# Performance work log

Measured on AMD Instinct MI355X. Metric: run time of the kernel, lower is better.

Reference implementation:

```python
import jax, jax.numpy as jnp
import numpy as np

D_MODEL = 4096
D_LATENT = 512
NUM_HEADS = 32
HEAD_DIM = D_MODEL // NUM_HEADS  # 128
ROPE_THETA = 10000.0
BATCH, SEQ = 2, 2048


def _rotate_half(x):
    x1, x2 = jnp.split(x, 2, axis=-1)
    return jnp.concatenate([-x2, x1], axis=-1)


def _rope_cos_sin(positions, head_dim, theta, dtype):
    # positions: [B, S] -> cos/sin: [B, S, 1, head_dim]
    inv_freq = 1.0 / (theta ** (jnp.arange(0, head_dim, 2, dtype=jnp.float32) / head_dim))
    freqs = positions.astype(jnp.float32)[..., None] * inv_freq  # [B,S,hd/2]
    emb = jnp.concatenate([freqs, freqs], axis=-1)               # [B,S,hd]
    return jnp.cos(emb)[:, :, None, :].astype(dtype), jnp.sin(emb)[:, :, None, :].astype(dtype)


def setup_inputs() -> dict:
    key = jax.random.key(0)
    ks = jax.random.split(key, 6)
    s = 0.02
    return {
        "hidden_states": jax.random.normal(ks[0], (BATCH, SEQ, D_MODEL), jnp.float32),
        "Wq": jax.random.normal(ks[1], (D_MODEL, NUM_HEADS * HEAD_DIM), jnp.float32) * s,
        "Wc": jax.random.normal(ks[2], (D_MODEL, D_LATENT), jnp.float32) * s,
        "Wk": jax.random.normal(ks[3], (D_LATENT, NUM_HEADS * HEAD_DIM), jnp.float32) * s,
        "Wv": jax.random.normal(ks[4], (D_LATENT, NUM_HEADS * HEAD_DIM), jnp.float32) * s,
        "Wo": jax.random.normal(ks[5], (NUM_HEADS * HEAD_DIM, D_MODEL), jnp.float32) * s,
    }


def reference(hidden_states, Wq, Wc, Wk, Wv, Wo):
    B, S, _ = hidden_states.shape
    H, Dh = NUM_HEADS, HEAD_DIM

    q = (hidden_states @ Wq).reshape(B, S, H, Dh)
    kv_latent = hidden_states @ Wc                     # [B,S,d_latent]
    k = (kv_latent @ Wk).reshape(B, S, H, Dh)
    v = (kv_latent @ Wv).reshape(B, S, H, Dh)

    # RoPE: q uses positions [0..S), k uses positions [0..S) (no past cache)
    pos = jnp.broadcast_to(jnp.arange(S)[None, :], (B, S))
    cos, sin = _rope_cos_sin(pos, Dh, ROPE_THETA, q.dtype)
    q = q * cos + _rotate_half(q) * sin
    k = k * cos + _rotate_half(k) * sin

    # standard attention, no mask (faithful to attention_mask=None path)
    scale = 1.0 / np.sqrt(Dh)
    scores = jnp.einsum("bqhd,bkhd->bhqk", q, k) * scale
    probs = jax.nn.softmax(scores, axis=-1)
    attn = jnp.einsum("bhqk,bkhd->bqhd", probs, v)     # [B,S,H,Dh]

    out = attn.reshape(B, S, H * Dh) @ Wo
    return out
```

## Files before the change

### kernel.cpp

```cpp
#include <hip/hip_runtime.h>
#include <hip/hip_bf16.h>
#include <cstdint>
#include <cstddef>

#define D_MODEL 4096
#define D_LATENT 512
#define NUM_HEADS 32
#define HEAD_DIM 128
#define BATCH 2
#define SEQ 2048
#define ROWS (BATCH*SEQ)

typedef __attribute__((ext_vector_type(8))) short bf16x8;
typedef __attribute__((ext_vector_type(4))) float f32x4;
typedef __attribute__((ext_vector_type(16))) float f32x16;
typedef unsigned int uint;

static __device__ __forceinline__ unsigned short f2bf(float f){
  union { float f; uint32_t u; } v; v.f = f;
  uint32_t r = (v.u + 0x7fffu + ((v.u >> 16) & 1u)) >> 16;
  return (unsigned short)r;
}
static __device__ __forceinline__ float bf2f(unsigned short h){
  union { uint32_t u; float f; } v; v.u = ((uint32_t)h) << 16;
  return v.f;
}
static __device__ __forceinline__ uint cvtpk(float lo, float hi2){
  uint r;
  asm("v_cvt_pk_bf16_f32 %0, %1, %2" : "=v"(r) : "v"(lo), "v"(hi2));
  return r;
}
static __device__ __forceinline__ void gload16(const void* g, void* l){
  __builtin_amdgcn_global_load_lds(
      (const __attribute__((address_space(1))) void*)g,
      (__attribute__((address_space(3))) void*)l, 16, 0, 0);
}

__global__ __launch_bounds__(256) void f32_to_bf16(
    const float* __restrict__ in, unsigned short* __restrict__ out){
  const size_t i = ((size_t)blockIdx.x * 256 + threadIdx.x) * 8;
  const float4 lo = *(const float4*)(in + i);
  const float4 hi = *(const float4*)(in + i + 4);
  uint4 d; unsigned short* dp = (unsigned short*)&d;
  dp[0]=f2bf(lo.x); dp[1]=f2bf(lo.y); dp[2]=f2bf(lo.z); dp[3]=f2bf(lo.w);
  dp[4]=f2bf(hi.x); dp[5]=f2bf(hi.y); dp[6]=f2bf(hi.z); dp[7]=f2bf(hi.w);
  *(uint4*)(out + i) = d;
}

__global__ __launch_bounds__(256) void transpose_convert(
    const float* __restrict__ W, unsigned short* __restrict__ Wt, int K, int N){
  __shared__ float tile[64][65];
  const int k0 = blockIdx.x * 64, n0 = blockIdx.y * 64;
  const int t = threadIdx.x;
  #pragma unroll
  for (int j = 0; j < 16; ++j){
    const int idx = t + 256*j;
    const int r = idx >> 6, c = idx & 63;
    tile[r][c] = W[(size_t)(k0 + r) * N + n0 + c];
  }
  __syncthreads();
  #pragma unroll
  for (int j = 0; j < 16; ++j){
    const int idx = t + 256*j;
    const int r = idx >> 6, c = idx & 63;
    Wt[(size_t)(n0 + r) * K + k0 + c] = f2bf(tile[c][r]);
  }
}

__global__ __launch_bounds__(256) void rope_table_kernel(float* __restrict__ ct,
                                                         float* __restrict__ st){
  const int i = blockIdx.x * 256 + threadIdx.x;
  if (i >= SEQ * 64) return;
  const int s = i >> 6, j = i & 63;
  const float inv = powf(10000.0f, -(float)j / 64.0f);
  const double a = (double)s * (double)inv;
  ct[i] = (float)cos(a);
  st[i] = (float)sin(a);
}

__global__ __launch_bounds__(256) void rope_apply(unsigned short* __restrict__ buf,
    const float* __restrict__ ct, const float* __restrict__ st, float scale){
  const int i = blockIdx.x * 256 + threadIdx.x;
  const int j = i & 63;
  const int tmp = i >> 6;
  const int h = tmp & 31;
  const int row = tmp >> 5;
  const int s = row & (SEQ - 1);
  const float c = ct[s*64 + j], sn = st[s*64 + j];
  const size_t base = (size_t)row * D_MODEL + (size_t)h * 128;
  const float x1 = bf2f(buf[base + j]);
  const float x2 = bf2f(buf[base + j + 64]);
  buf[base + j]      = f2bf((x1 * c - x2 * sn) * scale);
  buf[base + j + 64] = f2bf((x2 * c + x1 * sn) * scale);
}

template<bool OF32>
__global__ __launch_bounds__(256) void gemm_kernel(
    const unsigned short* __restrict__ A, const unsigned short* __restrict__ Bt,
    void* __restrict__ Cp, int M, int N, int K){
  __shared__ __align__(16) char As[128 * 128];
  __shared__ __align__(16) char Bs[128 * 128];
  const int t = threadIdx.x;
  const int nbx = gridDim.x;
  const int nwg = nbx * gridDim.y;
  int bid = blockIdx.y * nbx + blockIdx.x;
  bid = (bid & 7) * (nwg >> 3) + (bid >> 3);
  const int m0 = (bid / nbx) * 128, n0 = (bid % nbx) * 128;
  const int l = t & 63, wid = t >> 6;
  const int wr = wid >> 1, wcn = wid & 1;
  const int lr = l & 15, lg = l >> 4;

  const int srow = l >> 3;
  const int gch  = (l & 7) ^ srow;
  const unsigned short* gA = A  + (size_t)(m0 + wid*32 + srow) * K + gch*8;
  const unsigned short* gB = Bt + (size_t)(n0 + wid*32 + srow) * K + gch*8;
  char* lA = As + wid*4096;
  char* lB = Bs + wid*4096;

  f32x4 acc[4][4];
  #pragma unroll
  for (int i = 0; i < 4; ++i)
    #pragma unroll
    for (int j = 0; j < 4; ++j)
      #pragma unroll
      for (int r = 0; r < 4; ++r) acc[i][j][r] = 0.0f;

  const int kTiles = K >> 6;
  for (int kt = 0; kt < kTiles; ++kt){
    const size_t ko = (size_t)kt << 6;
    #pragma unroll
    for (int i = 0; i < 4; ++i){
      gload16(gA + (size_t)i*8*K + ko, lA + i*1024);
      gload16(gB + (size_t)i*8*K + ko, lB + i*1024);
    }
    __syncthreads();
    #pragma unroll
    for (int kc = 0; kc < 2; ++kc){
      bf16x8 af[4], bfv[4];
      const int ch = kc*4 + lg;
      #pragma unroll
      for (int mb = 0; mb < 4; ++mb){
        const int row = wr*64 + mb*16 + lr;
        af[mb] = *(const bf16x8*)(As + row*128 + ((ch ^ (row & 7)) * 16));
      }
      #pragma unroll
      for (int nb = 0; nb < 4; ++nb){
        const int row = wcn*64 + nb*16 + lr;
        bfv[nb] = *(const bf16x8*)(Bs + row*128 + ((ch ^ (row & 7)) * 16));
      }
      #pragma unroll
      for (int mb = 0; mb < 4; ++mb)
        #pragma unroll
        for (int nb = 0; nb < 4; ++nb)
          acc[mb][nb] = __builtin_amdgcn_mfma_f32_16x16x32_bf16(af[mb], bfv[nb], acc[mb][nb], 0, 0, 0);
    }
    __syncthreads();
  }
  #pragma unroll
  for (int mb = 0; mb < 4; ++mb)
    #pragma unroll
    for (int nb = 0; nb < 4; ++nb)
      #pragma unroll
      for (int r = 0; r < 4; ++r){
        const int row = m0 + wr*64 + mb*16 + lg*4 + r;
        const int col = n0 + wcn*64 + nb*16 + lr;
        if constexpr (OF32) ((float*)Cp)[(size_t)row * N + col] = acc[mb][nb][r];
        else ((unsigned short*)Cp)[(size_t)row * N + col] = f2bf(acc[mb][nb][r]);
      }
}

template<int MH>
static __device__ __forceinline__ void rdAh(bf16x8 (&a_)[4][2], const char* buf,
                                            int wr, int lr, int lg){
  #pragma unroll
  for (int mm = 0; mm < 4; ++mm)
    #pragma unroll
    for (int kc = 0; kc < 2; ++kc){
      const int row = wr*128 + (MH*4 + mm)*16 + lr;
      const int ch = kc*4 + lg;
      a_[mm][kc] = *(const bf16x8*)(buf + row*128 + ((ch ^ (row & 7)) * 16));
    }
}
template<int NH>
static __device__ __forceinline__ void rdBh(bf16x8 (&b_)[2][2][2], const char* buf,
                                            int wc, int lr, int lg){
  #pragma unroll
  for (int nn = 0; nn < 2; ++nn)
    #pragma unroll
    for (int kc = 0; kc < 2; ++kc){
      const int row = wc*64 + (NH*2 + nn)*16 + lr;
      const int ch = kc*4 + lg;
      b_[NH][nn][kc] = *(const bf16x8*)(buf + row*128 + ((ch ^ (row & 7)) * 16));
    }
}
template<int MH, int NH>
static __device__ __forceinline__ void mfq(f32x4 (&acc)[8][4],
    const bf16x8 (&a_)[4][2], const bf16x8 (&b_)[2][2][2]){
  __builtin_amdgcn_s_setprio(1);
  #pragma unroll
  for (int kc = 0; kc < 2; ++kc)
    #pragma unroll
    for (int mm = 0; mm < 4; ++mm)
      #pragma unroll
      for (int nn = 0; nn < 2; ++nn)
        acc[MH*4+mm][NH*2+nn] = __builtin_amdgcn_mfma_f32_16x16x32_bf16(
            a_[mm][kc], b_[NH][nn][kc], acc[MH*4+mm][NH*2+nn], 0, 0, 0);
  __builtin_amdgcn_s_setprio(0);
}

#define G256_BAR  __builtin_amdgcn_s_barrier()
#define G256_LGK0 do{ asm volatile("s_waitcnt lgkmcnt(0)" ::: "memory"); \
                      __builtin_amdgcn_sched_barrier(0); }while(0)
#define G256_VM(n) asm volatile("s_waitcnt vmcnt(" #n ")" ::: "memory")

template<bool OF32>
__global__ __launch_bounds__(512, 2) void gemm256_kernel(
    const unsigned short* __restrict__ A, const unsigned short* __restrict__ Bt,
    void* __restrict__ Cp, void* __restrict__ Cp2, int nsplit, int ldc, int ldc2,
    int M, int N, int K, int vt_mode){
  __shared__ __align__(16) char lds[131072];
  char* const As0 = lds;
  char* const As1 = lds + 32768;
  char* const Bs0 = lds + 65536;
  char* const Bs1 = lds + 98304;

  const int t = threadIdx.x;
  const int l = t & 63, wid = t >> 6;
  const int wr = wid >> 2, wc = wid & 3;
  const int lr = l & 15, lg = l >> 4;
  const int nbx = gridDim.x;
  const int nwg = nbx * gridDim.y;
  int bid = blockIdx.y * nbx + blockIdx.x;
  bid = (bid & 7) * (nwg >> 3) + (bid >> 3);
  const int m0 = (bid / nbx) * 256, n0 = (bid % nbx) * 256;

  const int srow = t >> 3;
  const int pch = t & 7;
  const int gch = pch ^ (srow & 7);
  const unsigned short* gAb = A  + (size_t)(m0 + srow) * K + gch*8;
  const unsigned short* gBb = Bt + (size_t)(n0 + srow) * K + gch*8;
  const int ldso = srow*128 + pch*16;

  auto stA = [&](char* dst, int half, int kcol){
    const unsigned short* g = gAb + (size_t)half*128*K + kcol;
    gload16(g,                dst + half*16384 + ldso);
    gload16(g + (size_t)64*K, dst + half*16384 + 8192 + ldso);
  };
  auto stB = [&](char* dst, int half, int kcol){
    const unsigned short* g = gBb + (size_t)half*128*K + kcol;
    gload16(g,                dst + half*16384 + ldso);
    gload16(g + (size_t)64*K, dst + half*16384 + 8192 + ldso);
  };

  f32x4 acc[8][4];
  #pragma unroll
  for (int m = 0; m < 8; ++m)
    #pragma unroll
    for (int n = 0; n < 4; ++n)
      #pragma unroll
      for (int r = 0; r < 4; ++r) acc[m][n][r] = 0.0f;
  bf16x8 a_[4][2];
  bf16x8 b_[2][2][2];

  const int niter = K >> 7;
  stA(As0, 0, 0); stA(As0, 1, 0); stB(Bs0, 0, 0); stB(Bs0, 1, 0);
  stA(As1, 0, 64);
  G256_VM(2);
  G256_BAR;
  __builtin_amdgcn_sched_barrier(0);

  for (int j = 0; j < niter; ++j){
    const int k0 = j << 7;
    const bool more = (j + 1 < niter);
    rdAh<0>(a_, As0, wr, lr, lg);
    rdBh<0>(b_, Bs0, wc, lr, lg);
    stA(As1, 1, k0 + 64);
    G256_BAR; G256_LGK0;
    mfq<0,0>(acc, a_, b_);
    G256_BAR;
    rdBh<1>(b_, Bs0, wc, lr, lg);
    stB(Bs1, 0, k0 + 64);
    G256_BAR; G256_LGK0;
    mfq<0,1>(acc, a_, b_);
    G256_BAR;
    rdAh<1>(a_, As0, wr, lr, lg);
    stB(Bs1, 1, k0 + 64);
    G256_BAR; G256_LGK0;
    mfq<1,0>(acc, a_, b_);
    G256_BAR;
    if (more){ stA(As0, 0, k0 + 128); G256_VM(2); }
    else     { G256_VM(0); }
    G256_BAR;
    __builtin_amdgcn_sched_barrier(0);
    mfq<1,1>(acc, a_, b_);
    G256_BAR;
    rdAh<0>(a_, As1, wr, lr, lg);
    rdBh<0>(b_, Bs1, wc, lr, lg);
    if (more) stA(As0, 1, k0 + 128);
    G256_BAR; G256_LGK0;
    mfq<0,0>(acc, a_, b_);
    G256_BAR;
    rdBh<1>(b_, Bs1, wc, lr, lg);
    if (more) stB(Bs0, 0, k0 + 128);
    G256_BAR; G256_LGK0;
    mfq<0,1>(acc, a_, b_);
    G256_BAR;
    rdAh<1>(a_, As1, wr, lr, lg);
    if (more) stB(Bs0, 1, k0 + 128);
    G256_BAR; G256_LGK0;
    mfq<1,0>(acc, a_, b_);
    G256_BAR;
    if (more){ stA(As1, 0, k0 + 192); G256_VM(2); }
    G256_BAR;
    __builtin_amdgcn_sched_barrier(0);
    mfq<1,1>(acc, a_, b_);
    G256_BAR;
  }

  if (n0 >= nsplit && vt_mode){
    unsigned short* vtp = (unsigned short*)Cp2;
    #pragma unroll
    for (int m = 0; m < 8; ++m)
      #pragma unroll
      for (int n = 0; n < 4; ++n)
        #pragma unroll
        for (int r = 0; r < 4; ++r){
          const int row = m0 + wr*128 + m*16 + lg*4 + r;
          const int col = (n0 - nsplit) + wc*64 + n*16 + lr;
          const size_t didx = ((size_t)(((row >> 11) << 5) | (col >> 7)) * 128
                               + (col & 127)) * SEQ + (row & (SEQ - 1));
          vtp[didx] = f2bf(acc[m][n][r]);
        }
    return;
  }
  void* outp = Cp;
  int c0 = n0, ld = ldc;
  if (n0 >= nsplit){ outp = Cp2; c0 = n0 - nsplit; ld = ldc2; }
  #pragma unroll
  for (int m = 0; m < 8; ++m)
    #pragma unroll
    for (int n = 0; n < 4; ++n)
      #pragma unroll
      for (int r = 0; r < 4; ++r){
        const int row = m0 + wr*128 + m*16 + lg*4 + r;
        const int col = c0 + wc*64 + n*16 + lr;
        if constexpr (OF32) ((float*)outp)[(size_t)row * ld + col] = acc[m][n][r];
        else ((unsigned short*)outp)[(size_t)row * ld + col] = f2bf(acc[m][n][r]);
      }
}

__global__ __launch_bounds__(512) void attn_kernel(
    const unsigned short* __restrict__ q, const unsigned short* __restrict__ kp,
    const unsigned short* __restrict__ vt, const float* __restrict__ ct,
    const float* __restrict__ st, unsigned short* __restrict__ o){
  __shared__ __align__(16) char Ks[2 * 16384];
  __shared__ __align__(16) char Vs[2 * 16384];
  const int t = threadIdx.x;
  const int l = t & 63, w = t >> 6;
  const int lq = l & 31, hi = l >> 5;
  const int bh = blockIdx.x, qb = blockIdx.y;
  const int b = bh >> 5;
  const size_t qbase = (size_t)b * SEQ + qb*256 + w*32;
  const size_t cb = (size_t)(bh & 31) * 128;

  auto stageK = [&](int buf, int kb){
    const size_t kr0 = (size_t)b * SEQ + (size_t)kb*64;
    char* kdst = Ks + buf*16384 + w*2048;
    #pragma unroll
    for (int i = 0; i < 2; ++i){
      const int r = w*8 + i*4 + (l >> 4);
      const int g = (l & 15) ^ (r & 15);
      gload16(kp + (kr0 + r) * D_MODEL + cb + g*8, kdst + i*1024);
    }
  };
  auto stageV = [&](int buf, int kb){
    char* vdst = Vs + buf*16384 + w*2048;
    #pragma unroll
    for (int i = 0; i < 2; ++i){
      const int r = w*16 + i*8 + (l >> 3);
      const int g = (l & 7) ^ (r & 7);
      gload16(vt + ((size_t)bh*128 + r) * SEQ + (size_t)kb*64 + g*8, vdst + i*1024);
    }
  };

  bf16x8 qf[8];
  #pragma unroll
  for (int dc = 0; dc < 8; ++dc)
    qf[dc] = *(const bf16x8*)(q + (qbase + lq) * D_MODEL + cb + dc*16 + hi*8);
  {
    const float qsc = 0.08838834764831845f * 1.4426950408889634f;
    const int s = qb*256 + w*32 + lq;
    #pragma unroll
    for (int dc = 0; dc < 4; ++dc){
      const int j0 = dc*16 + hi*8;
      const float4 c0 = *(const float4*)(ct + s*64 + j0);
      const float4 c1 = *(const float4*)(ct + s*64 + j0 + 4);
      const float4 s0_ = *(const float4*)(st + s*64 + j0);
      const float4 s1_ = *(const float4*)(st + s*64 + j0 + 4);
      const float cc[8] = {c0.x,c0.y,c0.z,c0.w,c1.x,c1.y,c1.z,c1.w};
      const float ss[8] = {s0_.x,s0_.y,s0_.z,s0_.w,s1_.x,s1_.y,s1_.z,s1_.w};
      #pragma unroll
      for (int e = 0; e < 8; ++e){
        const float x1 = bf2f((unsigned short)qf[dc][e]);
        const float x2 = bf2f((unsigned short)qf[dc + 4][e]);
        qf[dc][e]     = (short)f2bf((x1 * cc[e] - x2 * ss[e]) * qsc);
        qf[dc + 4][e] = (short)f2bf((x2 * cc[e] + x1 * ss[e]) * qsc);
      }
    }
  }

  f32x16 O[4];
  #pragma unroll
  for (int nb = 0; nb < 4; ++nb)
    #pragma unroll
    for (int r = 0; r < 16; ++r) O[nb][r] = 0.0f;
  float m = -1e30f, lsum = 0.0f;

  stageK(0, 0); stageV(0, 0);

  for (int kb = 0; kb < SEQ/64; ++kb){
    const bool more = (kb + 1 < SEQ/64);
    asm volatile("s_waitcnt vmcnt(0)" ::: "memory");
    __builtin_amdgcn_s_barrier();
    __builtin_amdgcn_sched_barrier(0);
    if (more){ stageK((kb + 1) & 1, kb + 1); stageV((kb + 1) & 1, kb + 1); }
    const char* Kb = Ks + (kb & 1)*16384;
    const char* Vb = Vs + (kb & 1)*16384;

    f32x16 s0, s1;
    #pragma unroll
    for (int r = 0; r < 16; ++r){ s0[r] = 0.0f; s1[r] = 0.0f; }
    __builtin_amdgcn_s_setprio(1);
    #pragma unroll
    for (int dc = 0; dc < 8; ++dc){
      const int ch = dc*2 + hi;
      const bf16x8 k0 = *(const bf16x8*)(Kb + lq*256 + ((ch ^ (lq & 15)) * 16));
      const bf16x8 k1 = *(const bf16x8*)(Kb + (32 + lq)*256 + ((ch ^ (lq & 15)) * 16));
      s0 = __builtin_amdgcn_mfma_f32_32x32x16_bf16(k0, qf[dc], s0, 0, 0, 0);
      s1 = __builtin_amdgcn_mfma_f32_32x32x16_bf16(k1, qf[dc], s1, 0, 0, 0);
    }
    __builtin_amdgcn_s_setprio(0);

    float mt = s0[0];
    #pragma unroll
    for (int r = 1; r < 16; ++r) mt = fmaxf(mt, s0[r]);
    #pragma unroll
    for (int r = 0; r < 16; ++r) mt = fmaxf(mt, s1[r]);
    mt = fmaxf(mt, __shfl_xor(mt, 32));

    if (!__all(mt <= m + 8.0f)){
      const float mnew = fmaxf(m, mt);
      const float al = __builtin_amdgcn_exp2f(m - mnew);
      m = mnew;
      lsum *= al;
      #pragma unroll
      for (int r = 0; r < 16; ++r){
        const int crow = (r & 3) + 8*(r >> 2) + 4*hi;
        const float albr = __shfl(al, crow);
        #pragma unroll
        for (int nb = 0; nb < 4; ++nb) O[nb][r] *= albr;
      }
    }

    float E[32];
    float sum = 0.0f;
    #pragma unroll
    for (int r = 0; r < 16; ++r){ E[r] = __builtin_amdgcn_exp2f(s0[r] - m); sum += E[r]; }
    #pragma unroll
    for (int r = 0; r < 16; ++r){ E[16 + r] = __builtin_amdgcn_exp2f(s1[r] - m); sum += E[16 + r]; }
    sum += __shfl_xor(sum, 32);
    lsum += sum;

    bf16x8 pa[4];
    #pragma unroll
    for (int c = 0; c < 4; ++c){
      const int rb = c * 8;
      const uint a_ = cvtpk(E[rb + 0], E[rb + 1]);
      const uint b_ = cvtpk(E[rb + 2], E[rb + 3]);
      const uint c_ = cvtpk(E[rb + 4], E[rb + 5]);
      const uint d_ = cvtpk(E[rb + 6], E[rb + 7]);
      const uint sa = (uint)__shfl_xor((int)a_, 32);
      const uint sb = (uint)__shfl_xor((int)b_, 32);
      const uint sc = (uint)__shfl_xor((int)c_, 32);
      const uint sd = (uint)__shfl_xor((int)d_, 32);
      union { uint u[4]; bf16x8 v; } uu;
      uu.u[0] = hi ? sc : a_;
      uu.u[1] = hi ? sd : b_;
      uu.u[2] = hi ? c_ : sa;
      uu.u[3] = hi ? d_ : sb;
      pa[c] = uu.v;
    }

    __builtin_amdgcn_s_setprio(1);
    #pragma unroll
    for (int c = 0; c < 4; ++c){
      const int ch = c*2 + hi;
      #pragma unroll
      for (int nb = 0; nb < 4; ++nb){
        const int vr = nb*32 + lq;
        const bf16x8 vf = *(const bf16x8*)(Vb + vr*128 + ((ch ^ (vr & 7)) * 16));
        O[nb] = __builtin_amdgcn_mfma_f32_32x32x16_bf16(pa[c], vf, O[nb], 0, 0, 0);
      }
    }
    __builtin_amdgcn_s_setprio(0);
  }

  const float rinv = 1.0f / lsum;
  #pragma unroll
  for (int r = 0; r < 16; ++r){
    const int crow = (r & 3) + 8*(r >> 2) + 4*hi;
    const float rb_ = __shfl(rinv, crow);
    #pragma unroll
    for (int nb = 0; nb < 4; ++nb)
      o[(qbase + crow) * D_MODEL + cb + nb*32 + lq] = f2bf(O[nb][r] * rb_);
  }
}

extern "C" void kernel_launch(void* const* d_in, const int* in_sizes, int n_in,
                              void* d_out, int out_size, void* d_ws, size_t ws_size,
                              hipStream_t stream){
  const float* hidden = (const float*)d_in[0];
  const float* Wq = (const float*)d_in[1];
  const float* Wc = (const float*)d_in[2];
  const float* Wk = (const float*)d_in[3];
  const float* Wv = (const float*)d_in[4];
  const float* Wo = (const float*)d_in[5];
  float* out = (float*)d_out;

  char* ws = (char*)d_ws;
  size_t off = 0;
  auto alloc = [&](size_t bytes)->char*{
    char* p = ws + off; off += (bytes + 255) & ~(size_t)255; return p;
  };
  unsigned short* Wqt  = (unsigned short*)alloc((size_t)D_MODEL * D_MODEL * 2);
  unsigned short* Wct  = (unsigned short*)alloc((size_t)D_LATENT * D_MODEL * 2);
  unsigned short* Wkvt = (unsigned short*)alloc((size_t)2 * D_MODEL * D_LATENT * 2);
  unsigned short* Wot  = (unsigned short*)alloc((size_t)D_MODEL * D_MODEL * 2);
  unsigned short* latent = (unsigned short*)alloc((size_t)ROWS * D_LATENT * 2);
  unsigned short* qbuf = (unsigned short*)alloc((size_t)ROWS * D_MODEL * 2);
  unsigned short* kbuf = (unsigned short*)alloc((size_t)ROWS * D_MODEL * 2);
  unsigned short* attnb= (unsigned short*)alloc((size_t)ROWS * D_MODEL * 2);
  float* ctab = (float*)alloc((size_t)SEQ * 64 * 4);
  float* stab = (float*)alloc((size_t)SEQ * 64 * 4);
  unsigned short* hbf   = attnb;
  unsigned short* vtbuf = Wqt;

  const dim3 B256(256);

  f32_to_bf16<<<(ROWS*(size_t)D_MODEL)/2048, B256, 0, stream>>>(hidden, hbf);
  transpose_convert<<<dim3(64, 64), B256, 0, stream>>>(Wq, Wqt, D_MODEL, D_MODEL);
  transpose_convert<<<dim3(64, 8),  B256, 0, stream>>>(Wc, Wct, D_MODEL, D_LATENT);
  transpose_convert<<<dim3(8, 64),  B256, 0, stream>>>(Wk, Wkvt, D_LATENT, D_MODEL);
  transpose_convert<<<dim3(8, 64),  B256, 0, stream>>>(Wv, Wkvt + (size_t)D_MODEL*D_LATENT, D_LATENT, D_MODEL);
  transpose_convert<<<dim3(64, 64), B256, 0, stream>>>(Wo, Wot, D_MODEL, D_MODEL);
  rope_table_kernel<<<512, B256, 0, stream>>>(ctab, stab);

  gemm_kernel<false><<<dim3(D_LATENT/128, ROWS/128), B256, 0, stream>>>(
      hbf, Wct, latent, ROWS, D_LATENT, D_MODEL);
  gemm256_kernel<false><<<dim3(D_MODEL/256, ROWS/256), dim3(512), 0, stream>>>(
      hbf, Wqt, qbuf, qbuf, 1 << 30, D_MODEL, D_MODEL, ROWS, D_MODEL, D_MODEL, 0);
  gemm256_kernel<false><<<dim3(2*D_MODEL/256, ROWS/256), dim3(512), 0, stream>>>(
      latent, Wkvt, kbuf, vtbuf, D_MODEL, D_MODEL, 0, ROWS, 2*D_MODEL, D_LATENT, 1);

  rope_apply<<<(ROWS * NUM_HEADS * 64) / 256, B256, 0, stream>>>(kbuf, ctab, stab, 1.0f);

  attn_kernel<<<dim3(BATCH * NUM_HEADS, SEQ/256), dim3(512), 0, stream>>>(
      qbuf, kbuf, vtbuf, ctab, stab, attnb);

  gemm256_kernel<true><<<dim3(D_MODEL/256, ROWS/256), dim3(512), 0, stream>>>(
      attnb, Wot, out, out, 1 << 30, D_MODEL, D_MODEL, ROWS, D_MODEL, D_MODEL, 0);
}
```

Before: 609.6 us.

## Split-K the latent projection GEMM and batch weight transposes into fewer launches

```diff
diff --git a/kernel.cpp b/kernel.cpp
--- a/kernel.cpp
+++ b/kernel.cpp
@@ -45,6 +45,30 @@
   dp[0]=f2bf(lo.x); dp[1]=f2bf(lo.y); dp[2]=f2bf(lo.z); dp[3]=f2bf(lo.w);
   dp[4]=f2bf(hi.x); dp[5]=f2bf(hi.y); dp[6]=f2bf(hi.z); dp[7]=f2bf(hi.w);
   *(uint4*)(out + i) = d;
+}
+
+__global__ __launch_bounds__(256) void transpose_convert2(
+    const float* __restrict__ S0, unsigned short* __restrict__ D0,
+    const float* __restrict__ S1, unsigned short* __restrict__ D1,
+    int K, int N){
+  __shared__ float tile[64][65];
+  const float* W = blockIdx.z ? S1 : S0;
+  unsigned short* Wt = blockIdx.z ? D1 : D0;
+  const int k0 = blockIdx.x * 64, n0 = blockIdx.y * 64;
+  const int t = threadIdx.x;
+  #pragma unroll
+  for (int j = 0; j < 16; ++j){
+    const int idx = t + 256*j;
+    const int r = idx >> 6, c = idx & 63;
+    tile[r][c] = W[(size_t)(k0 + r) * N + n0 + c];
+  }
+  __syncthreads();
+  #pragma unroll
+  for (int j = 0; j < 16; ++j){
+    const int idx = t + 256*j;
+    const int r = idx >> 6, c = idx & 63;
+    Wt[(size_t)(n0 + r) * K + k0 + c] = f2bf(tile[c][r]);
+  }
 }
 
 __global__ __launch_bounds__(256) void transpose_convert(
@@ -94,13 +118,13 @@
   buf[base + j + 64] = f2bf((x2 * c + x1 * sn) * scale);
 }
 
-template<bool OF32>
-__global__ __launch_bounds__(256) void gemm_kernel(
+__global__ __launch_bounds__(256) void gemm_splitk_kernel(
     const unsigned short* __restrict__ A, const unsigned short* __restrict__ Bt,
-    void* __restrict__ Cp, int M, int N, int K){
+    float* __restrict__ Cpart, int M, int N, int Kfull, int Kpart){
   __shared__ __align__(16) char As[128 * 128];
   __shared__ __align__(16) char Bs[128 * 128];
   const int t = threadIdx.x;
+  const int kz = blockIdx.z;
   const int nbx = gridDim.x;
   const int nwg = nbx * gridDim.y;
   int bid = blockIdx.y * nbx + blockIdx.x;
@@ -112,8 +136,9 @@
 
   const int srow = l >> 3;
   const int gch  = (l & 7) ^ srow;
-  const unsigned short* gA = A  + (size_t)(m0 + wid*32 + srow) * K + gch*8;
-  const unsigned short* gB = Bt + (size_t)(n0 + wid*32 + srow) * K + gch*8;
+  const size_t kofs = (size_t)kz * Kpart;
+  const unsigned short* gA = A  + (size_t)(m0 + wid*32 + srow) * Kfull + kofs + gch*8;
+  const unsigned short* gB = Bt + (size_t)(n0 + wid*32 + srow) * Kfull + kofs + gch*8;
   char* lA = As + wid*4096;
   char* lB = Bs + wid*4096;
 
@@ -125,13 +150,13 @@
       #pragma unroll
       for (int r = 0; r < 4; ++r) acc[i][j][r] = 0.0f;
 
-  const int kTiles = K >> 6;
+  const int kTiles = Kpart >> 6;
   for (int kt = 0; kt < kTiles; ++kt){
     const size_t ko = (size_t)kt << 6;
     #pragma unroll
     for (int i = 0; i < 4; ++i){
-      gload16(gA + (size_t)i*8*K + ko, lA + i*1024);
-      gload16(gB + (size_t)i*8*K + ko, lB + i*1024);
+      gload16(gA + (size_t)i*8*Kfull + ko, lA + i*1024);
+      gload16(gB + (size_t)i*8*Kfull + ko, lB + i*1024);
     }
     __syncthreads();
     #pragma unroll
@@ -156,6 +181,7 @@
     }
     __syncthreads();
   }
+  float* Cp = Cpart + (size_t)kz * M * N;
   #pragma unroll
   for (int mb = 0; mb < 4; ++mb)
     #pragma unroll
@@ -164,9 +190,21 @@
       for (int r = 0; r < 4; ++r){
         const int row = m0 + wr*64 + mb*16 + lg*4 + r;
         const int col = n0 + wcn*64 + nb*16 + lr;
-        if constexpr (OF32) ((float*)Cp)[(size_t)row * N + col] = acc[mb][nb][r];
-        else ((unsigned short*)Cp)[(size_t)row * N + col] = f2bf(acc[mb][nb][r]);
+        Cp[(size_t)row * N + col] = acc[mb][nb][r];
       }
+}
+
+__global__ __launch_bounds__(256) void latent_reduce(
+    const float* __restrict__ p, unsigned short* __restrict__ out, size_t n){
+  const size_t i = ((size_t)blockIdx.x * 256 + threadIdx.x) * 8;
+  const float4 a0 = *(const float4*)(p + i);
+  const float4 a1 = *(const float4*)(p + i + 4);
+  const float4 b0 = *(const float4*)(p + n + i);
+  const float4 b1 = *(const float4*)(p + n + i + 4);
+  uint4 d; unsigned short* dp = (unsigned short*)&d;
+  dp[0]=f2bf(a0.x+b0.x); dp[1]=f2bf(a0.y+b0.y); dp[2]=f2bf(a0.z+b0.z); dp[3]=f2bf(a0.w+b0.w);
+  dp[4]=f2bf(a1.x+b1.x); dp[5]=f2bf(a1.y+b1.y); dp[6]=f2bf(a1.z+b1.z); dp[7]=f2bf(a1.w+b1.w);
+  *(uint4*)(out + i) = d;
 }
 
 template<int MH>
@@ -540,6 +578,7 @@
   unsigned short* qbuf = (unsigned short*)alloc((size_t)ROWS * D_MODEL * 2);
   unsigned short* kbuf = (unsigned short*)alloc((size_t)ROWS * D_MODEL * 2);
   unsigned short* attnb= (unsigned short*)alloc((size_t)ROWS * D_MODEL * 2);
+  float* lpart = (float*)alloc((size_t)2 * ROWS * D_LATENT * 4);
   float* ctab = (float*)alloc((size_t)SEQ * 64 * 4);
   float* stab = (float*)alloc((size_t)SEQ * 64 * 4);
   unsigned short* hbf   = attnb;
@@ -548,15 +587,17 @@
   const dim3 B256(256);
 
   f32_to_bf16<<<(ROWS*(size_t)D_MODEL)/2048, B256, 0, stream>>>(hidden, hbf);
-  transpose_convert<<<dim3(64, 64), B256, 0, stream>>>(Wq, Wqt, D_MODEL, D_MODEL);
-  transpose_convert<<<dim3(64, 8),  B256, 0, stream>>>(Wc, Wct, D_MODEL, D_LATENT);
-  transpose_convert<<<dim3(8, 64),  B256, 0, stream>>>(Wk, Wkvt, D_LATENT, D_MODEL);
-  transpose_convert<<<dim3(8, 64),  B256, 0, stream>>>(Wv, Wkvt + (size_t)D_MODEL*D_LATENT, D_LATENT, D_MODEL);
-  transpose_convert<<<dim3(64, 64), B256, 0, stream>>>(Wo, Wot, D_MODEL, D_MODEL);
+  transpose_convert2<<<dim3(64, 64, 2), B256, 0, stream>>>(Wq, Wqt, Wo, Wot, D_MODEL, D_MODEL);
+  transpose_convert2<<<dim3(8, 64, 2),  B256, 0, stream>>>(
+      Wk, Wkvt, Wv, Wkvt + (size_t)D_MODEL*D_LATENT, D_LATENT, D_MODEL);
+  transpose_convert<<<dim3(64, 8), B256, 0, stream>>>(Wc, Wct, D_MODEL, D_LATENT);
   rope_table_kernel<<<512, B256, 0, stream>>>(ctab, stab);
 
-  gemm_kernel<false><<<dim3(D_LATENT/128, ROWS/128), B256, 0, stream>>>(
-      hbf, Wct, latent, ROWS, D_LATENT, D_MODEL);
+  gemm_splitk_kernel<<<dim3(D_LATENT/128, ROWS/128, 2), B256, 0, stream>>>(
+      hbf, Wct, lpart, ROWS, D_LATENT, D_MODEL, D_MODEL/2);
+  latent_reduce<<<(ROWS*(size_t)D_LATENT)/2048, B256, 0, stream>>>(
+      lpart, latent, (size_t)ROWS * D_LATENT);
+
   gemm256_kernel<false><<<dim3(D_MODEL/256, ROWS/256), dim3(512), 0, stream>>>(
       hbf, Wqt, qbuf, qbuf, 1 << 30, D_MODEL, D_MODEL, ROWS, D_MODEL, D_MODEL, 0);
   gemm256_kernel<false><<<dim3(2*D_MODEL/256, ROWS/256), dim3(512), 0, stream>>>(
```

Measured after the change: 578.0 us. 1.05x faster.
